# Kernel tuning notes

Hardware: AMD Instinct MI355X
Metric: run time of the kernel (lower is better)

The kernel has to match this reference:

```python
import jax, jax.numpy as jnp
import numpy as np
import math

B, S, E, H = 2, 2048, 2048, 16
HD = E // H // 2  # 64, per-head dim of each differential half
DEPTH = 12
LAMBDA_INIT = 0.8 - 0.6 * math.exp(-0.3 * DEPTH)
EPS = 1e-5


def setup_inputs() -> dict:
    key = jax.random.key(0)
    ks = jax.random.split(key, 10)
    sc = 0.02
    return {
        "x": jax.random.normal(ks[0], (B, S, E), jnp.float32),
        "Wq": jax.random.normal(ks[1], (E, E), jnp.float32) * sc,
        "Wk": jax.random.normal(ks[2], (E, E), jnp.float32) * sc,
        "Wv": jax.random.normal(ks[3], (E, E), jnp.float32) * sc,
        "Wo": jax.random.normal(ks[4], (E, E), jnp.float32) * sc,
        "lambda_q1": jax.random.normal(ks[5], (HD,), jnp.float32) * 0.1,
        "lambda_k1": jax.random.normal(ks[6], (HD,), jnp.float32) * 0.1,
        "lambda_q2": jax.random.normal(ks[7], (HD,), jnp.float32) * 0.1,
        "lambda_k2": jax.random.normal(ks[8], (HD,), jnp.float32) * 0.1,
        "gamma": jnp.ones((2 * HD,), jnp.float32),
    }


def _rope_interleaved(x, cos, sin):
    # x: [b, s, h, d]; cos/sin: [s, d//2]; pairs are (0,1),(2,3),...
    xe, xo = x[..., 0::2], x[..., 1::2]
    c = cos[None, :, None, :]
    s = sin[None, :, None, :]
    oe = xe * c - xo * s
    oo = xe * s + xo * c
    return jnp.stack([oe, oo], axis=-1).reshape(x.shape)


def reference(x, Wq, Wk, Wv, Wo, lambda_q1, lambda_k1, lambda_q2, lambda_k2, gamma):
    b, t, _ = x.shape
    # rotary tables (rotary dim == HD, interleaved)
    angle = 1.0 / 10000 ** jnp.linspace(0.0, 1.0, HD // 2, dtype=jnp.float32)
    freqs = jnp.arange(t, dtype=jnp.float32)[:, None] * angle  # [t, HD//2]
    cos, sin = jnp.cos(freqs), jnp.sin(freqs)

    q = (x @ Wq.T).reshape(b, t, 2 * H, HD)
    k = (x @ Wk.T).reshape(b, t, 2 * H, HD)
    v = (x @ Wv.T).reshape(b, t, H, 2 * HD)  # concat(v1, v2) along last dim

    q = _rope_interleaved(q, cos, sin)
    k = _rope_interleaved(k, cos, sin)

    q = q.reshape(b, t, H, 2, HD)
    k = k.reshape(b, t, H, 2, HD)
    q1, q2 = q[:, :, :, 0], q[:, :, :, 1]
    k1, k2 = k[:, :, :, 0], k[:, :, :, 1]

    scale = HD ** -0.5  # flash_attn default softmax scale
    # branch 1: softmax(q1 k1) @ [v1|v2]
    s1 = jnp.einsum("bthd,bshd->bhts", q1, k1) * scale
    p1 = jax.nn.softmax(s1, axis=-1)
    o1 = jnp.einsum("bhts,bshd->bthd", p1, v)  # [b,t,H,2*HD]
    # branch 2: softmax(q2 k2) @ [v1|v2]
    s2 = jnp.einsum("bthd,bshd->bhts", q2, k2) * scale
    p2 = jax.nn.softmax(s2, axis=-1)
    o2 = jnp.einsum("bhts,bshd->bthd", p2, v)

    lam1 = jnp.exp(jnp.sum(lambda_q1 * lambda_k1))
    lam2 = jnp.exp(jnp.sum(lambda_q2 * lambda_k2))
    lam = lam1 - lam2 + LAMBDA_INIT

    attn = o1 - lam * o2  # [b,t,H,2*HD]
    # RMSNorm over last dim (2*HD) with affine gamma
    rms = jax.lax.rsqrt(jnp.mean(attn * attn, axis=-1, keepdims=True) + EPS)
    attn = attn * rms * gamma
    attn = attn * (1.0 - LAMBDA_INIT)
    attn = attn.reshape(b, t, H * 2 * HD)
    return attn @ Wo.T
```

## Files before the change

kernel.cpp:

```cpp
#include <hip/hip_runtime.h>
#include <cstdint>
#include <cstddef>

typedef unsigned short u16;
typedef __attribute__((ext_vector_type(8))) short short8;
typedef __attribute__((ext_vector_type(4))) float f32x4;

#define MFMA_B16(a,b,c) __builtin_amdgcn_mfma_f32_16x16x32_bf16((a),(b),(c),0,0,0)

#define S_LEN 2048
#define EMB 2048
#define QKV_N 6144
#define HD 64
#define LAMBDA_INIT_F 0.78360576653162f
#define ONE_MINUS_LI 0.21639423346838f

static __device__ __forceinline__ u16 f2bf(float f) {
  unsigned u = __float_as_uint(f);
  unsigned r = ((u >> 16) & 1u) + 0x7fffu;
  return (u16)((u + r) >> 16);
}
static __device__ __forceinline__ float bf2f(u16 h) {
  return __uint_as_float(((unsigned)h) << 16);
}
static __device__ __forceinline__ void gload_lds16(const u16* g, u16* l) {
  __builtin_amdgcn_global_load_lds((const __attribute__((address_space(1))) void*)g,
                                   (__attribute__((address_space(3))) void*)l, 16, 0, 0);
}

__global__ void cvt_f32_bf16(const float* __restrict__ s, u16* __restrict__ d, int n4) {
  int i = blockIdx.x * 256 + threadIdx.x;
  if (i >= n4) return;
  f32x4 v = *(const f32x4*)&s[i * 4];
  unsigned long long pk = (unsigned long long)f2bf(v[0])
                        | ((unsigned long long)f2bf(v[1]) << 16)
                        | ((unsigned long long)f2bf(v[2]) << 32)
                        | ((unsigned long long)f2bf(v[3]) << 48);
  *(unsigned long long*)&d[i * 4] = pk;
}

template <int BF16OUT>
__global__ __launch_bounds__(256, 2) void gemm_bt(const u16* __restrict__ A,
                                                  const u16* __restrict__ B,
                                                  void* __restrict__ Cout,
                                                  int M, int N, int K) {
  __shared__ u16 As[128 * 32];
  __shared__ u16 Bs[128 * 32];
  const int tid = threadIdx.x;
  const int lane = tid & 63, wv = tid >> 6;
  const int bm = blockIdx.x * 128, bn = blockIdx.y * 128;
  const int wr = (wv >> 1) * 64, wc = (wv & 1) * 64;
  const int lr = lane & 15, hk = lane >> 4;

  const int r0 = tid >> 2;
  const int c0 = (tid & 3) * 8;
  const u16* ga = A + (size_t)(bm + r0) * K + c0;
  const u16* gb = B + (size_t)(bn + r0) * K + c0;
  const size_t rstep = (size_t)64 * K;

  f32x4 acc[4][4] = {};

  for (int k0 = 0; k0 < K; k0 += 32) {
    __syncthreads();
    gload_lds16(ga + k0,         &As[(tid) * 8]);
    gload_lds16(ga + rstep + k0, &As[(tid + 256) * 8]);
    gload_lds16(gb + k0,         &Bs[(tid) * 8]);
    gload_lds16(gb + rstep + k0, &Bs[(tid + 256) * 8]);
    __syncthreads();
    short8 af[4], bfv[4];
#pragma unroll
    for (int i = 0; i < 4; i++) af[i] = *(const short8*)&As[(wr + i * 16 + lr) * 32 + hk * 8];
#pragma unroll
    for (int j = 0; j < 4; j++) bfv[j] = *(const short8*)&Bs[(wc + j * 16 + lr) * 32 + hk * 8];
#pragma unroll
    for (int i = 0; i < 4; i++)
#pragma unroll
      for (int j = 0; j < 4; j++)
        acc[i][j] = MFMA_B16(af[i], bfv[j], acc[i][j]);
  }

  if (BF16OUT) {
    u16* C = (u16*)Cout;
#pragma unroll
    for (int i = 0; i < 4; i++)
#pragma unroll
      for (int j = 0; j < 4; j++)
#pragma unroll
        for (int r = 0; r < 4; r++) {
          int row = bm + wr + i * 16 + hk * 4 + r;
          int col = bn + wc + j * 16 + lr;
          C[(size_t)row * N + col] = f2bf(acc[i][j][r]);
        }
  } else {
    float* C = (float*)Cout;
#pragma unroll
    for (int i = 0; i < 4; i++)
#pragma unroll
      for (int j = 0; j < 4; j++)
#pragma unroll
        for (int r = 0; r < 4; r++) {
          int row = bm + wr + i * 16 + hk * 4 + r;
          int col = bn + wc + j * 16 + lr;
          C[(size_t)row * N + col] = acc[i][j][r];
        }
  }
}

__global__ void rope_kernel(u16* __restrict__ qkv) {
  int idx = blockIdx.x * 256 + threadIdx.x;
  int p = idx & 31;
  int u = (idx >> 5) & 63;
  int m = idx >> 11;
  int t = m & (S_LEN - 1);
  int col = (u < 32) ? (u * 64 + 2 * p) : (EMB + (u - 32) * 64 + 2 * p);
  u16* ptr = qkv + (size_t)m * QKV_N + col;
  unsigned v = *(unsigned*)ptr;
  float xe = bf2f((u16)(v & 0xffff));
  float xo = bf2f((u16)(v >> 16));
  float w = expf((float)p * (-9.210340371976184f / 31.0f));
  float ang = (float)t * w;
  float sn, cs;
  sincosf(ang, &sn, &cs);
  float oe = xe * cs - xo * sn;
  float oo = xe * sn + xo * cs;
  *(unsigned*)ptr = (unsigned)f2bf(oe) | (((unsigned)f2bf(oo)) << 16);
}

#define LDP 88

__global__ __launch_bounds__(256, 2) void attn_kernel(
    const u16* __restrict__ qkv, u16* __restrict__ attnb,
    const float* __restrict__ lq1, const float* __restrict__ lk1,
    const float* __restrict__ lq2, const float* __restrict__ lk2,
    const float* __restrict__ gamma) {
  __shared__ u16 K1s[64 * LDP];
  __shared__ u16 K2s[64 * LDP];
  __shared__ u16 VTs[128 * LDP];
  __shared__ u16 Ps[4 * 2 * 16 * LDP];

  const int g = blockIdx.x;
  const int xcd = g & 7;
  const int gi = g >> 3;
  const int bh = xcd * 4 + (gi >> 5);
  const int qt = gi & 31;
  const int b = bh >> 4, h = bh & 15;

  const int tid = threadIdx.x, lane = tid & 63, wv = tid >> 6;
  const int lr = lane & 15, hk = lane >> 4;

  float d1 = 0.f, d2 = 0.f;
  for (int d = 0; d < HD; d++) { d1 += lq1[d] * lk1[d]; d2 += lq2[d] * lk2[d]; }
  const float lam = __expf(d1) - __expf(d2) + LAMBDA_INIT_F;

  const int qrow = qt * 64 + wv * 16 + lr;
  const u16* qp = qkv + (size_t)(b * S_LEN + qrow) * QKV_N;
  short8 q1f[2], q2f[2];
  q1f[0] = *(const short8*)&qp[(2 * h) * 64 + hk * 8];
  q1f[1] = *(const short8*)&qp[(2 * h) * 64 + 32 + hk * 8];
  q2f[0] = *(const short8*)&qp[(2 * h + 1) * 64 + hk * 8];
  q2f[1] = *(const short8*)&qp[(2 * h + 1) * 64 + 32 + hk * 8];

  f32x4 o1a[8] = {};
  f32x4 o2a[8] = {};
  float l1p = 0.f, l2p = 0.f;

  const int sr = tid >> 3;
  const int scc = (tid & 7) * 8;
  const int vkv = (tid & 31) * 2;
  const int vd0 = (tid >> 5) * 8;

  const u16* kb1 = qkv + (size_t)b * S_LEN * QKV_N + EMB + (2 * h) * 64;
  const u16* kb2 = kb1 + 64;
  const u16* vbp = qkv + (size_t)b * S_LEN * QKV_N + 2 * EMB + h * 128;

  u16* P1 = &Ps[(wv * 2 + 0) * 16 * LDP];
  u16* P2 = &Ps[(wv * 2 + 1) * 16 * LDP];

  for (int kv0 = 0; kv0 < S_LEN; kv0 += 64) {
    __syncthreads();
#pragma unroll
    for (int ps = 0; ps < 2; ps++) {
      int r = sr + ps * 32;
      const u16* s1 = kb1 + (size_t)(kv0 + r) * QKV_N + scc;
      const u16* s2 = kb2 + (size_t)(kv0 + r) * QKV_N + scc;
      *(short8*)&K1s[r * LDP + scc] = *(const short8*)s1;
      *(short8*)&K2s[r * LDP + scc] = *(const short8*)s2;
    }
#pragma unroll
    for (int ps = 0; ps < 2; ps++) {
      int d0 = vd0 + ps * 64;
      const u16* vs = vbp + (size_t)(kv0 + vkv) * QKV_N + d0;
      short8 va = *(const short8*)vs;
      short8 vb8 = *(const short8*)(vs + QKV_N);
#pragma unroll
      for (int j = 0; j < 8; j++) {
        unsigned pk = (unsigned)(u16)va[j] | (((unsigned)(u16)vb8[j]) << 16);
        *(unsigned*)&VTs[(d0 + j) * LDP + vkv] = pk;
      }
    }
    __syncthreads();

#pragma unroll
    for (int st = 0; st < 2; st++) {
      const u16* Ks = st ? K2s : K1s;
      const short8* qf = st ? q2f : q1f;
      u16* Pw = st ? P2 : P1;
      float lacc = 0.f;
#pragma unroll
      for (int kt = 0; kt < 4; kt++) {
        f32x4 s = {0.f, 0.f, 0.f, 0.f};
        short8 ka0 = *(const short8*)&Ks[(kt * 16 + lr) * LDP + hk * 8];
        short8 ka1 = *(const short8*)&Ks[(kt * 16 + lr) * LDP + 32 + hk * 8];
        s = MFMA_B16(ka0, qf[0], s);
        s = MFMA_B16(ka1, qf[1], s);
        float e0 = __expf(s[0] * 0.125f);
        float e1 = __expf(s[1] * 0.125f);
        float e2 = __expf(s[2] * 0.125f);
        float e3 = __expf(s[3] * 0.125f);
        lacc += (e0 + e1) + (e2 + e3);
        unsigned long long pk = (unsigned long long)f2bf(e0)
                              | ((unsigned long long)f2bf(e1) << 16)
                              | ((unsigned long long)f2bf(e2) << 32)
                              | ((unsigned long long)f2bf(e3) << 48);
        *(unsigned long long*)&Pw[lr * LDP + kt * 16 + hk * 4] = pk;
      }
      if (st) l2p += lacc; else l1p += lacc;
    }
    asm volatile("" ::: "memory");

    short8 p10 = *(const short8*)&P1[lr * LDP + hk * 8];
    short8 p11 = *(const short8*)&P1[lr * LDP + 32 + hk * 8];
    short8 p20 = *(const short8*)&P2[lr * LDP + hk * 8];
    short8 p21 = *(const short8*)&P2[lr * LDP + 32 + hk * 8];
#pragma unroll
    for (int dt = 0; dt < 8; dt++) {
      short8 va0 = *(const short8*)&VTs[(dt * 16 + lr) * LDP + hk * 8];
      short8 va1 = *(const short8*)&VTs[(dt * 16 + lr) * LDP + 32 + hk * 8];
      o1a[dt] = MFMA_B16(va0, p10, o1a[dt]);
      o1a[dt] = MFMA_B16(va1, p11, o1a[dt]);
      o2a[dt] = MFMA_B16(va0, p20, o2a[dt]);
      o2a[dt] = MFMA_B16(va1, p21, o2a[dt]);
    }
  }

  float l1 = l1p; l1 += __shfl_xor(l1, 16); l1 += __shfl_xor(l1, 32);
  float l2 = l2p; l2 += __shfl_xor(l2, 16); l2 += __shfl_xor(l2, 32);
  const float inv1 = 1.f / l1;
  const float inv2 = 1.f / l2;

  float av[8][4];
  float ss = 0.f;
#pragma unroll
  for (int dt = 0; dt < 8; dt++)
#pragma unroll
    for (int r = 0; r < 4; r++) {
      float a = o1a[dt][r] * inv1 - lam * (o2a[dt][r] * inv2);
      av[dt][r] = a;
      ss += a * a;
    }
  ss += __shfl_xor(ss, 16); ss += __shfl_xor(ss, 32);
  const float sc2 = rsqrtf(ss * (1.f / 128.f) + 1e-5f) * ONE_MINUS_LI;

  u16* orow = attnb + (size_t)(b * S_LEN + qrow) * EMB + h * 128;
#pragma unroll
  for (int dt = 0; dt < 8; dt++) {
    int d = dt * 16 + hk * 4;
    f32x4 gv = *(const f32x4*)&gamma[d];
    unsigned long long pk = (unsigned long long)f2bf(av[dt][0] * gv[0] * sc2)
                          | ((unsigned long long)f2bf(av[dt][1] * gv[1] * sc2) << 16)
                          | ((unsigned long long)f2bf(av[dt][2] * gv[2] * sc2) << 32)
                          | ((unsigned long long)f2bf(av[dt][3] * gv[3] * sc2) << 48);
    *(unsigned long long*)&orow[d] = pk;
  }
}

extern "C" void kernel_launch(void* const* d_in, const int* in_sizes, int n_in,
                              void* d_out, int out_size, void* d_ws, size_t ws_size,
                              hipStream_t stream) {
  (void)in_sizes; (void)n_in; (void)out_size; (void)ws_size;
  const float* x   = (const float*)d_in[0];
  const float* Wq  = (const float*)d_in[1];
  const float* Wk  = (const float*)d_in[2];
  const float* Wv  = (const float*)d_in[3];
  const float* Wo  = (const float*)d_in[4];
  const float* lq1 = (const float*)d_in[5];
  const float* lk1 = (const float*)d_in[6];
  const float* lq2 = (const float*)d_in[7];
  const float* lk2 = (const float*)d_in[8];
  const float* gam = (const float*)d_in[9];

  char* ws = (char*)d_ws;
  u16* xb    = (u16*)(ws);
  u16* Wcat  = (u16*)(ws + 16777216);
  u16* Wob   = (u16*)(ws + 41943040);
  u16* qkv   = (u16*)(ws + 50331648);
  u16* attnb = xb;

  const int NE = EMB * EMB;
  cvt_f32_bf16<<<(2 * NE / 4 + 255) / 256, 256, 0, stream>>>(x, xb, 2 * NE / 4);
  cvt_f32_bf16<<<(NE / 4 + 255) / 256, 256, 0, stream>>>(Wq, Wcat, NE / 4);
  cvt_f32_bf16<<<(NE / 4 + 255) / 256, 256, 0, stream>>>(Wk, Wcat + NE, NE / 4);
  cvt_f32_bf16<<<(NE / 4 + 255) / 256, 256, 0, stream>>>(Wv, Wcat + 2 * NE, NE / 4);
  cvt_f32_bf16<<<(NE / 4 + 255) / 256, 256, 0, stream>>>(Wo, Wob, NE / 4);

  dim3 g1(4096 / 128, QKV_N / 128);
  gemm_bt<1><<<g1, 256, 0, stream>>>(xb, Wcat, qkv, 4096, QKV_N, EMB);

  rope_kernel<<<(4096 * 64 * 32) / 256, 256, 0, stream>>>(qkv);

  attn_kernel<<<1024, 256, 0, stream>>>(qkv, attnb, lq1, lk1, lq2, lk2, gam);

  dim3 g2(4096 / 128, EMB / 128);
  gemm_bt<0><<<g2, 256, 0, stream>>>(attnb, Wob, d_out, 4096, EMB, EMB);
}
```

Measured before the change: 391.2 us.

## Prefetch next K/V tile into registers and XOR-swizzle LDS in attention kernel

The attention kernel now loads the next K1/K2/V tile from global memory into registers while the current tile is being computed, which hides global load latency behind the MFMA work. The padded LDS layout (stride 88) is replaced by an unpadded 128-byte-row layout with an XOR swizzle, so shared memory drops and bank conflicts are still avoided. Launch bounds go from 2 to 3 blocks per SM, and the lambda dot product becomes a wave-level shuffle reduction instead of a serial loop. The prefetch registers and the higher occupancy target both add register pressure, which could cause spills.

```diff
diff --git a/kernel.cpp b/kernel.cpp
--- a/kernel.cpp
+++ b/kernel.cpp
@@ -126,17 +126,17 @@
   *(unsigned*)ptr = (unsigned)f2bf(oe) | (((unsigned)f2bf(oo)) << 16);
 }
 
-#define LDP 88
-
-__global__ __launch_bounds__(256, 2) void attn_kernel(
+#define SW(row, colByte) ((((row)) << 7) + ((colByte) ^ (((row) & 7) << 4)))
+
+__global__ __launch_bounds__(256, 3) void attn_kernel(
     const u16* __restrict__ qkv, u16* __restrict__ attnb,
     const float* __restrict__ lq1, const float* __restrict__ lk1,
     const float* __restrict__ lq2, const float* __restrict__ lk2,
     const float* __restrict__ gamma) {
-  __shared__ u16 K1s[64 * LDP];
-  __shared__ u16 K2s[64 * LDP];
-  __shared__ u16 VTs[128 * LDP];
-  __shared__ u16 Ps[4 * 2 * 16 * LDP];
+  __shared__ u16 K1s[64 * 64];
+  __shared__ u16 K2s[64 * 64];
+  __shared__ u16 VTs[128 * 64];
+  __shared__ u16 Ps[4 * 2 * 16 * 64];
 
   const int g = blockIdx.x;
   const int xcd = g & 7;
@@ -148,8 +148,10 @@
   const int tid = threadIdx.x, lane = tid & 63, wv = tid >> 6;
   const int lr = lane & 15, hk = lane >> 4;
 
-  float d1 = 0.f, d2 = 0.f;
-  for (int d = 0; d < HD; d++) { d1 += lq1[d] * lk1[d]; d2 += lq2[d] * lk2[d]; }
+  float d1 = lq1[lane] * lk1[lane];
+  float d2 = lq2[lane] * lk2[lane];
+#pragma unroll
+  for (int off = 32; off; off >>= 1) { d1 += __shfl_xor(d1, off); d2 += __shfl_xor(d2, off); }
   const float lam = __expf(d1) - __expf(d2) + LAMBDA_INIT_F;
 
   const int qrow = qt * 64 + wv * 16 + lr;
@@ -173,44 +175,57 @@
   const u16* kb2 = kb1 + 64;
   const u16* vbp = qkv + (size_t)b * S_LEN * QKV_N + 2 * EMB + h * 128;
 
-  u16* P1 = &Ps[(wv * 2 + 0) * 16 * LDP];
-  u16* P2 = &Ps[(wv * 2 + 1) * 16 * LDP];
+  char* P1 = (char*)&Ps[(wv * 2 + 0) * 16 * 64];
+  char* P2 = (char*)&Ps[(wv * 2 + 1) * 16 * 64];
+  char* K1c = (char*)K1s;
+  char* K2c = (char*)K2s;
+  char* VTc = (char*)VTs;
+
+  short8 rk1[2], rk2[2], rv0[2], rv1[2];
+
+#define LOADT(kv0_)                                                              \
+  {                                                                              \
+    _Pragma("unroll") for (int ps = 0; ps < 2; ps++) {                           \
+      int r = sr + ps * 32;                                                      \
+      rk1[ps] = *(const short8*)(kb1 + (size_t)((kv0_) + r) * QKV_N + scc);      \
+      rk2[ps] = *(const short8*)(kb2 + (size_t)((kv0_) + r) * QKV_N + scc);      \
+      const u16* vs = vbp + (size_t)((kv0_) + vkv) * QKV_N + vd0 + ps * 64;      \
+      rv0[ps] = *(const short8*)vs;                                              \
+      rv1[ps] = *(const short8*)(vs + QKV_N);                                    \
+    }                                                                            \
+  }
+
+  LOADT(0);
 
   for (int kv0 = 0; kv0 < S_LEN; kv0 += 64) {
     __syncthreads();
 #pragma unroll
     for (int ps = 0; ps < 2; ps++) {
       int r = sr + ps * 32;
-      const u16* s1 = kb1 + (size_t)(kv0 + r) * QKV_N + scc;
-      const u16* s2 = kb2 + (size_t)(kv0 + r) * QKV_N + scc;
-      *(short8*)&K1s[r * LDP + scc] = *(const short8*)s1;
-      *(short8*)&K2s[r * LDP + scc] = *(const short8*)s2;
-    }
-#pragma unroll
-    for (int ps = 0; ps < 2; ps++) {
+      *(short8*)(K1c + SW(r, scc * 2)) = rk1[ps];
+      *(short8*)(K2c + SW(r, scc * 2)) = rk2[ps];
       int d0 = vd0 + ps * 64;
-      const u16* vs = vbp + (size_t)(kv0 + vkv) * QKV_N + d0;
-      short8 va = *(const short8*)vs;
-      short8 vb8 = *(const short8*)(vs + QKV_N);
 #pragma unroll
       for (int j = 0; j < 8; j++) {
-        unsigned pk = (unsigned)(u16)va[j] | (((unsigned)(u16)vb8[j]) << 16);
-        *(unsigned*)&VTs[(d0 + j) * LDP + vkv] = pk;
+        unsigned pk = (unsigned)(u16)rv0[ps][j] | (((unsigned)(u16)rv1[ps][j]) << 16);
+        *(unsigned*)(VTc + SW(d0 + j, vkv * 2)) = pk;
       }
     }
+    if (kv0 + 64 < S_LEN) LOADT(kv0 + 64);
     __syncthreads();
 
 #pragma unroll
     for (int st = 0; st < 2; st++) {
-      const u16* Ks = st ? K2s : K1s;
+      const char* Ks = st ? K2c : K1c;
       const short8* qf = st ? q2f : q1f;
-      u16* Pw = st ? P2 : P1;
+      char* Pw = st ? P2 : P1;
       float lacc = 0.f;
 #pragma unroll
       for (int kt = 0; kt < 4; kt++) {
         f32x4 s = {0.f, 0.f, 0.f, 0.f};
-        short8 ka0 = *(const short8*)&Ks[(kt * 16 + lr) * LDP + hk * 8];
-        short8 ka1 = *(const short8*)&Ks[(kt * 16 + lr) * LDP + 32 + hk * 8];
+        int row = kt * 16 + lr;
+        short8 ka0 = *(const short8*)(Ks + SW(row, hk * 16));
+        short8 ka1 = *(const short8*)(Ks + SW(row, 64 + hk * 16));
         s = MFMA_B16(ka0, qf[0], s);
         s = MFMA_B16(ka1, qf[1], s);
         float e0 = __expf(s[0] * 0.125f);
@@ -222,26 +237,28 @@
                               | ((unsigned long long)f2bf(e1) << 16)
                               | ((unsigned long long)f2bf(e2) << 32)
                               | ((unsigned long long)f2bf(e3) << 48);
-        *(unsigned long long*)&Pw[lr * LDP + kt * 16 + hk * 4] = pk;
+        *(unsigned long long*)(Pw + SW(lr, kt * 32 + hk * 8)) = pk;
       }
       if (st) l2p += lacc; else l1p += lacc;
     }
     asm volatile("" ::: "memory");
 
-    short8 p10 = *(const short8*)&P1[lr * LDP + hk * 8];
-    short8 p11 = *(const short8*)&P1[lr * LDP + 32 + hk * 8];
-    short8 p20 = *(const short8*)&P2[lr * LDP + hk * 8];
-    short8 p21 = *(const short8*)&P2[lr * LDP + 32 + hk * 8];
+    short8 p10 = *(const short8*)(P1 + SW(lr, hk * 16));
+    short8 p11 = *(const short8*)(P1 + SW(lr, 64 + hk * 16));
+    short8 p20 = *(const short8*)(P2 + SW(lr, hk * 16));
+    short8 p21 = *(const short8*)(P2 + SW(lr, 64 + hk * 16));
 #pragma unroll
     for (int dt = 0; dt < 8; dt++) {
-      short8 va0 = *(const short8*)&VTs[(dt * 16 + lr) * LDP + hk * 8];
-      short8 va1 = *(const short8*)&VTs[(dt * 16 + lr) * LDP + 32 + hk * 8];
+      int row = dt * 16 + lr;
+      short8 va0 = *(const short8*)(VTc + SW(row, hk * 16));
+      short8 va1 = *(const short8*)(VTc + SW(row, 64 + hk * 16));
       o1a[dt] = MFMA_B16(va0, p10, o1a[dt]);
       o1a[dt] = MFMA_B16(va1, p11, o1a[dt]);
       o2a[dt] = MFMA_B16(va0, p20, o2a[dt]);
       o2a[dt] = MFMA_B16(va1, p21, o2a[dt]);
     }
   }
+#undef LOADT
 
   float l1 = l1p; l1 += __shfl_xor(l1, 16); l1 += __shfl_xor(l1, 32);
   float l2 = l2p; l2 += __shfl_xor(l2, 16); l2 += __shfl_xor(l2, 32);
```

New measurement: 535.3 us. 36.8% more time.
